# Optimization experiments

Measured on AMD Instinct MI355X. Metric: run time of the kernel, lower is better.

Reference implementation:

```python
import jax, jax.numpy as jnp
import numpy as np

L = 6                      # lmax = mmax (single resolution)
C = 128                    # sphere_channels
H = 256                    # hidden_channels
EC = 128                   # edge_channels
NG = 512                   # gaussian distance basis size
NC = (L + 1) ** 2          # 49 spherical coefficients
GP = 2 * (L + 1) ** 2      # 98 grid points
N_ATOMS = 800
N_EDGES = 8000
MAX_ELEM = 90
CUTOFF = 8.0
M_SIZES = [L - m + 1 for m in range(L + 1)]
MAXIN = L * C              # widest per-m SO2 input (m=1)


def _perm_np():
    # l-primary index of coefficient (l, m) is l*l + l + m
    idx = lambda l, m: l * l + l + m
    p = [idx(l, 0) for l in range(L + 1)]
    for m in range(1, L + 1):
        p += [idx(l, -m) for l in range(m, L + 1)]
        p += [idx(l, m) for l in range(m, L + 1)]
    return np.array(p)

_P = _perm_np()
PERM = jnp.array(_P)          # l-primary -> m-primary (x._m_primary)
INV_PERM = jnp.array(np.argsort(_P))  # m-primary -> l-primary (x._l_primary)


def silu(x):
    return x * jax.nn.sigmoid(x)


def setup_inputs() -> dict:
    key = jax.random.key(0)
    ks = iter(jax.random.split(key, 64))
    def nrm(shape, scale):
        return jax.random.normal(next(ks), shape, dtype=jnp.float32) * np.float32(scale)
    def lin(out_d, in_d):
        return nrm((out_d, in_d), 1.0 / np.sqrt(in_d))
    def so2_params(prefix):
        return {
            prefix + 'w_dist0': lin(H, EC), prefix + 'b_dist0': jnp.zeros((H,), jnp.float32),
            prefix + 'w1_m0': lin(H, M_SIZES[0] * C), prefix + 'w2_m0': lin(M_SIZES[0] * C, H),
            prefix + 'wdist_m': nrm((L, 2 * H, EC), 1.0 / np.sqrt(EC)),
            prefix + 'bdist_m': jnp.zeros((L, 2 * H), jnp.float32),
            prefix + 'w1r': nrm((L, H, MAXIN), 1.0 / np.sqrt(MAXIN)),
            prefix + 'w2r': nrm((L, MAXIN, H), 1.0 / np.sqrt(H)),
            prefix + 'w1i': nrm((L, H, MAXIN), 1.0 / np.sqrt(MAXIN)),
            prefix + 'w2i': nrm((L, MAXIN, H), 1.0 / np.sqrt(H)),
        }
    inp = dict(
        x=nrm((N_ATOMS, NC, C), 1.0),
        edge_distance=jax.random.uniform(next(ks), (N_EDGES,), jnp.float32, 0.5, CUTOFF),
        wigner=nrm((N_EDGES, NC, NC), 1.0 / np.sqrt(NC)),
        wigner_inv=nrm((N_EDGES, NC, NC), 1.0 / np.sqrt(NC)),
        to_grid_mat=nrm((GP, NC), 1.0 / np.sqrt(NC)),
        from_grid_mat=nrm((NC, GP), 1.0 / np.sqrt(GP)),
        w_dist1=lin(EC, NG), b_dist1=jnp.zeros((EC,), jnp.float32),
        src_emb=jax.random.uniform(next(ks), (MAX_ELEM, EC), jnp.float32, -0.001, 0.001),
        tgt_emb=jax.random.uniform(next(ks), (MAX_ELEM, EC), jnp.float32, -0.001, 0.001),
        w_edge1=lin(EC, EC), b_edge1=jnp.zeros((EC,), jnp.float32),
        ws1=lin(C, 2 * C), bs1=jnp.zeros((C,), jnp.float32),
        ws2=lin(C, C), bs2=jnp.zeros((C,), jnp.float32),
        ws3=lin(C, C), bs3=jnp.zeros((C,), jnp.float32),
        atomic_numbers=jax.random.randint(next(ks), (N_ATOMS,), 0, MAX_ELEM),
        edge_index=jax.random.randint(next(ks), (2, N_EDGES), 0, N_ATOMS),
    )
    inp.update(so2_params('s_'))
    inp.update(so2_params('t_'))
    return inp


def _so2_block(xr, x_edge, p):
    # SO2Block: m-primary reorder, m=0 gated MLP, per-m complex gated GEMMs, back to l-primary
    (w_dist0, b_dist0, w1_m0, w2_m0, wdist_m, bdist_m, w1r, w2r, w1i, w2i) = p
    E = xr.shape[0]
    xm = xr[:, PERM]                                   # [E, NC, C] m-primary
    n0 = M_SIZES[0]
    g0 = silu(x_edge @ w_dist0.T + b_dist0)            # [E, H]
    x0 = xm[:, :n0].reshape(E, n0 * C)
    x0 = ((x0 @ w1_m0.T) * g0) @ w2_m0.T
    outs = [x0.reshape(E, n0, C)]
    off = n0
    for m in range(1, L + 1):
        n = M_SIZES[m]; k = n * C
        blk = xm[:, off:off + 2 * n].reshape(E, 2, k)  # [E, 2(real/imag), n*C]
        ge = silu(x_edge @ wdist_m[m - 1].T + bdist_m[m - 1]).reshape(E, 2, H)
        xr_ = jnp.einsum('eik,hk->eih', blk, w1r[m - 1, :, :k]) * ge[:, 0:1]
        xr_ = jnp.einsum('eih,kh->eik', xr_, w2r[m - 1, :k])
        xi_ = jnp.einsum('eik,hk->eih', blk, w1i[m - 1, :, :k]) * ge[:, 1:2]
        xi_ = jnp.einsum('eih,kh->eik', xi_, w2i[m - 1, :k])
        out = jnp.stack([xr_[:, 0] - xi_[:, 1], xr_[:, 1] + xi_[:, 0]], axis=1)
        outs.append(out.reshape(E, 2 * n, C))
        off += 2 * n
    return jnp.concatenate(outs, axis=1)[:, INV_PERM]


def reference(x, edge_distance, wigner, wigner_inv, to_grid_mat, from_grid_mat,
              w_dist1, b_dist1, src_emb, tgt_emb, w_edge1, b_edge1,
              s_w_dist0, s_b_dist0, s_w1_m0, s_w2_m0, s_wdist_m, s_bdist_m,
              s_w1r, s_w2r, s_w1i, s_w2i,
              t_w_dist0, t_b_dist0, t_w1_m0, t_w2_m0, t_wdist_m, t_bdist_m,
              t_w1r, t_w2r, t_w1i, t_w2i,
              ws1, bs1, ws2, bs2, ws3, bs3,
              atomic_numbers, edge_index):
    # --- EdgeBlock ---
    offsets = jnp.linspace(0.0, CUTOFF, NG)
    coeff = np.float32(-0.5 / (CUTOFF / (NG - 1)) ** 2)
    basis = jnp.exp(coeff * (edge_distance[:, None] - offsets) ** 2)   # GaussianSmearing
    x_dist = basis @ w_dist1.T + b_dist1
    x_edge = silu(src_emb[atomic_numbers[edge_index[0]]]
                  + tgt_emb[atomic_numbers[edge_index[1]]] + x_dist)
    x_edge = silu(x_edge @ w_edge1.T + b_edge1)                        # [E, EC]
    # --- gather per-edge embeddings and rotate into edge frame ---
    x_src = jnp.einsum('eij,ejc->eic', wigner, x[edge_index[0]])
    x_tgt = jnp.einsum('eij,ejc->eic', wigner, x[edge_index[1]])
    # --- SO2 blocks ---
    x_src = _so2_block(x_src, x_edge, (s_w_dist0, s_b_dist0, s_w1_m0, s_w2_m0,
                                       s_wdist_m, s_bdist_m, s_w1r, s_w2r, s_w1i, s_w2i))
    x_tgt = _so2_block(x_tgt, x_edge, (t_w_dist0, t_b_dist0, t_w1_m0, t_w2_m0,
                                       t_wdist_m, t_bdist_m, t_w1r, t_w2r, t_w1i, t_w2i))
    msg = x_src + x_tgt
    # --- grid activation (x._grid_act) ---
    g = silu(jnp.einsum('gi,eic->egc', to_grid_mat, msg))
    msg = jnp.einsum('ig,egc->eic', from_grid_mat, g)
    # --- rotate back and aggregate (x._rotate_inv, x._reduce_edge) ---
    msg = jnp.einsum('eij,ejc->eic', wigner_inv, msg)
    x_msg = jax.ops.segment_sum(msg, edge_index[1], num_segments=x.shape[0])
    # --- LayerBlock point-wise spherical nonlinearity on the grid ---
    gx = jnp.einsum('gi,nic->ngc', to_grid_mat, x)
    gm = jnp.einsum('gi,nic->ngc', to_grid_mat, x_msg)
    g = jnp.concatenate([gx, gm], axis=-1)            # [N, GP, 2C]
    g = silu(g @ ws1.T + bs1)
    g = silu(g @ ws2.T + bs2)
    g = g @ ws3.T + bs3
    return jnp.einsum('ig,ngc->nic', from_grid_mat, g)
```

## Files before the change

### kernel.cpp

```cpp
#include <hip/hip_runtime.h>
#include <string.h>

#define EN 8000
#define AN 800

typedef __attribute__((ext_vector_type(8))) short bf16x8;
typedef __attribute__((ext_vector_type(4))) float f32x4;
typedef unsigned short ushort_t;
typedef unsigned int uint32;

__constant__ int c_perm[49] = {
  0,2,6,12,20,30,42,
  1,5,11,19,29,41,
  3,7,13,21,31,43,
  4,10,18,28,40,
  8,14,22,32,44,
  9,17,27,39,
  15,23,33,45,
  16,26,38,
  24,34,46,
  25,37,
  35,47,
  36,
  48
};

__device__ __forceinline__ float siluf(float x) { return x / (1.0f + __expf(-x)); }
__device__ __forceinline__ ushort_t f2bf(float f) {
  uint32 u = __float_as_uint(f);
  u += 0x7fff + ((u >> 16) & 1);
  return (ushort_t)(u >> 16);
}
__device__ __forceinline__ float bf2f(ushort_t h) {
  return __uint_as_float(((uint32)h) << 16);
}
__device__ __forceinline__ void gld16(const void* g, void* l) {
  __builtin_amdgcn_global_load_lds(
      (const __attribute__((address_space(1))) void*)g,
      (__attribute__((address_space(3))) void*)l, 16, 0, 0);
}

__global__ __launch_bounds__(256) void k_build_b2b(
    const float* __restrict__ sw2r, const float* __restrict__ sw2i,
    const float* __restrict__ tw2r, const float* __restrict__ tw2i,
    ushort_t* __restrict__ dst)
{
  long long id = (long long)blockIdx.x * 256 + threadIdx.x;
  if (id >= 5505024LL) return;
  long long base = 0; int m = 1, k = 768;
  for (; m <= 6; ++m) {
    k = (7 - m) * 128;
    long long sz = 2LL * k * 1024;
    if (id < base + sz) break;
    base += sz;
  }
  long long rem = id - base;
  int p = (int)(rem / ((long long)k * 1024));
  int cj = (int)(rem - (long long)p * k * 1024);
  int c = cj >> 10, j = cj & 1023;
  int q = j >> 8, jj = j & 255;
  const float sgn = (q & 1) ? (p ? 1.f : -1.f) : 1.f;
  const float* src = (q < 2) ? (q == 0 ? sw2r : sw2i) : (q == 2 ? tw2r : tw2i);
  dst[id] = f2bf(sgn * src[(long long)(m - 1) * 196608 + c * 256 + jj]);
}

__global__ __launch_bounds__(256) void k_build_bgcat(
    const float* __restrict__ sw0, const float* __restrict__ tw0,
    const float* __restrict__ sw4, const float* __restrict__ tw4,
    const float* __restrict__ sb0, const float* __restrict__ tb0b,
    const float* __restrict__ sbd, const float* __restrict__ tbd,
    ushort_t* __restrict__ w, float* __restrict__ b)
{
  int id = blockIdx.x * 256 + threadIdx.x;
  if (id < 851968) {
    int r = id >> 7, c = id & 127;
    float v;
    if (r < 256) v = sw0[r * 128 + c];
    else if (r < 512) v = tw0[(r - 256) * 128 + c];
    else {
      int rr = r - 512, m = rr >> 10, q = rr & 1023;
      v = (q < 512) ? sw4[m * 65536 + q * 128 + c] : tw4[m * 65536 + (q - 512) * 128 + c];
    }
    w[id] = f2bf(v);
    return;
  }
  id -= 851968;
  if (id < 6656) {
    float v;
    if (id < 256) v = sb0[id];
    else if (id < 512) v = tb0b[id - 256];
    else {
      int rr = id - 512, m = rr >> 10, q = rr & 1023;
      v = (q < 512) ? sbd[m * 512 + q] : tbd[m * 512 + (q - 512)];
    }
    b[id] = v;
  }
}

__global__ __launch_bounds__(256) void k_build_b20b(
    const float* __restrict__ sw3, const float* __restrict__ tw3,
    ushort_t* __restrict__ b20)
{
  int id = blockIdx.x * 256 + threadIdx.x;
  if (id >= 458752) return;
  int cc = id >> 9, j = id & 511;
  b20[id] = f2bf((j < 256) ? sw3[cc * 256 + j] : tw3[cc * 256 + (j - 256)]);
}

__global__ __launch_bounds__(256) void k_build_s1m(
    const float* __restrict__ sw6, const float* __restrict__ sw8,
    const float* __restrict__ tw6, const float* __restrict__ tw8,
    ushort_t* __restrict__ dst)
{
  long long id = (long long)blockIdx.x * 256 + threadIdx.x;
  if (id >= 2752512LL) return;
  long long base = 0; int m = 1, k = 768;
  for (; m <= 6; ++m) {
    k = (7 - m) * 128;
    long long sz = 1024LL * k;
    if (id < base + sz) break;
    base += sz;
  }
  long long rem = id - base;
  int s = (int)(rem / (512LL * k));
  int rr = (int)(rem - (long long)s * 512 * k);
  int r = rr / k, c = rr - r * k;
  const float* src = (r < 256) ? (s ? tw6 : sw6) : (s ? tw8 : sw8);
  int r0 = (r < 256) ? r : r - 256;
  dst[id] = f2bf(src[(long long)(m - 1) * 196608 + r0 * 768 + c]);
}

__global__ __launch_bounds__(256) void k_cvt(
    const float* __restrict__ src, ushort_t* __restrict__ dst, int n)
{
  int id = blockIdx.x * 256 + threadIdx.x;
  if (id < n) dst[id] = f2bf(src[id]);
}

__global__ __launch_bounds__(256) void k_build_tg(
    const float* __restrict__ tg, ushort_t* __restrict__ dst)
{
  int id = blockIdx.x * 256 + threadIdx.x;
  if (id >= 98 * 49) return;
  int r = id / 49, s = id - r * 49;
  dst[id] = f2bf(tg[r * 49 + c_perm[s]]);
}

__global__ __launch_bounds__(256) void k_xT(
    const float* __restrict__ x, ushort_t* __restrict__ xbT)
{
  __shared__ __align__(16) float xs[49 * 128];
  const int a = blockIdx.x, t = threadIdx.x;
  const float4* src = (const float4*)(x + (long long)a * 6272);
  float4* d = (float4*)xs;
  for (int i = t; i < 1568; i += 256) d[i] = src[i];
  __syncthreads();
  ushort_t* o = xbT + (long long)a * 8192;
  int c = t >> 1;
  int jg = (t & 1) << 2;
  #pragma unroll
  for (int u = 0; u < 4; ++u) {
    int g = jg + u;
    bf16x8 v = (bf16x8)0;
    #pragma unroll
    for (int j = 0; j < 8; ++j) {
      int jj = (g << 3) + j;
      if (jj < 49) v[j] = (short)f2bf(xs[jj * 128 + c]);
    }
    *(bf16x8*)&o[(c << 6) + (g << 3)] = v;
  }
}

__global__ __launch_bounds__(256) void k_basis(
    const float* __restrict__ dist, ushort_t* __restrict__ basis)
{
  int id = blockIdx.x * 256 + threadIdx.x;
  if (id >= EN * 512) return;
  int e = id >> 9, g = id & 511;
  const float step = 8.0f / 511.0f;
  const float coeff = -2040.0078125f;
  float df = dist[e] - (float)g * step;
  basis[id] = f2bf(expf(coeff * df * df));
}

__global__ __launch_bounds__(256) void k_emb(
    const float* __restrict__ src_emb, const float* __restrict__ tgt_emb,
    const int* __restrict__ anum, const int* __restrict__ eidx,
    const float* __restrict__ xd, ushort_t* __restrict__ out)
{
  int id = blockIdx.x * 256 + threadIdx.x;
  if (id >= EN * 128) return;
  int e = id >> 7, c = id & 127;
  int a0 = anum[eidx[e]], a1 = anum[eidx[EN + e]];
  out[id] = f2bf(siluf(src_emb[a0 * 128 + c] + tgt_emb[a1 * 128 + c] + xd[id]));
}

__global__ __launch_bounds__(256) void k_rot2(
    const float* __restrict__ wig, const ushort_t* __restrict__ xbT,
    const int* __restrict__ srcl, const int* __restrict__ tgtl,
    ushort_t* __restrict__ osrc, ushort_t* __restrict__ otgt)
{
  __shared__ short Ws[4096];
  __shared__ short Xs[8192];
  __shared__ short Xt[8192];
  const int e = blockIdx.x, tid = threadIdx.x;
  const int lane = tid & 63, wave = tid >> 6;
  const float* wge = wig + (long long)e * 2401;
  #pragma unroll
  for (int t = 0; t < 2; ++t) {
    int ci = (t << 8) + tid;
    int row = ci >> 3, g = ci & 7;
    bf16x8 v = (bf16x8)0;
    if (row < 49) {
      const float* wr = wge + c_perm[row] * 49;
      #pragma unroll
      for (int j = 0; j < 8; ++j) {
        int col = (g << 3) + j;
        if (col < 49) v[j] = (short)f2bf(wr[col]);
      }
    }
    *(bf16x8*)&Ws[(row << 6) + ((g ^ (row & 7)) << 3)] = v;
  }
  const int as = srcl[e], at = tgtl[e];
  const ushort_t* xsg = xbT + (long long)as * 8192;
  const ushort_t* xtg = xbT + (long long)at * 8192;
  #pragma unroll
  for (int t = 0; t < 4; ++t) {
    int ci = (t << 8) + tid;
    int row = ci >> 3, g = ci & 7;
    int ofs = (row << 6) + ((g ^ (row & 7)) << 3);
    *(bf16x8*)&Xs[ofs] = *(const bf16x8*)&xsg[ci << 3];
    *(bf16x8*)&Xt[ofs] = *(const bf16x8*)&xtg[ci << 3];
  }
  __syncthreads();
  const short* Xb = (wave >> 1) ? Xt : Xs;
  const int ch = (wave & 1) << 6;
  const int fr = lane & 15, g = lane >> 4;
  f32x4 acc[4][4];
  #pragma unroll
  for (int i = 0; i < 4; ++i)
    #pragma unroll
    for (int j = 0; j < 4; ++j) acc[i][j] = (f32x4){0.f, 0.f, 0.f, 0.f};
  #pragma unroll
  for (int ks = 0; ks < 2; ++ks) {
    bf16x8 af[4], bfv[4];
    int lc = (ks << 2) + g;
    #pragma unroll
    for (int i = 0; i < 4; ++i) {
      int ra = (i << 4) + fr;
      af[i] = *(const bf16x8*)&Ws[(ra << 6) + ((lc ^ (ra & 7)) << 3)];
      int rb = ch + (i << 4) + fr;
      bfv[i] = *(const bf16x8*)&Xb[(rb << 6) + ((lc ^ (rb & 7)) << 3)];
    }
    #pragma unroll
    for (int i = 0; i < 4; ++i)
      #pragma unroll
      for (int j = 0; j < 4; ++j)
        acc[i][j] = __builtin_amdgcn_mfma_f32_16x16x32_bf16(af[i], bfv[j], acc[i][j], 0, 0, 0);
  }
  const int crl = (lane >> 4) << 2, ccl = lane & 15;
  __syncthreads();
  short* Ob = (wave >> 1) ? Xt : Xs;
  #pragma unroll
  for (int i = 0; i < 4; ++i)
    #pragma unroll
    for (int r = 0; r < 4; ++r) {
      int q = (i << 4) + crl + r;
      if (q < 49) {
        #pragma unroll
        for (int j = 0; j < 4; ++j) {
          int col = ch + (j << 4) + ccl;
          Ob[(q << 7) + (((col >> 3) ^ (q & 15)) << 3) + (col & 7)] =
              (short)f2bf(acc[i][j][r]);
        }
      }
    }
  __syncthreads();
  for (int gid = tid; gid < 1568; gid += 256) {
    int half = gid >= 784;
    int c784 = half ? gid - 784 : gid;
    int row = c784 >> 4, cc = c784 & 15;
    const short* Sb = half ? Xt : Xs;
    bf16x8 v = *(const bf16x8*)&Sb[(row << 7) + ((cc ^ (row & 15)) << 3)];
    ushort_t* dst = (half ? otgt : osrc) + (long long)e * 6272 + (row << 7) + (cc << 3);
    *(bf16x8*)dst = v;
  }
}

struct GemmP {
  const ushort_t* A; const ushort_t* A2; const ushort_t* B;
  const float* bias; const ushort_t* gate; void* C;
  int a_se, a_si, pair, asplit;
  int ldb;
  int gate_ofs;
  int c_se, c_si, c_ofs;
  int ihalf, act, c_bf16;
  int M, N, K;
  int ngx, wg_base;
};
struct Grouped { GemmP d[14]; int nd; int nwg; };

__global__ __launch_bounds__(256) void gemm_g(Grouped G) {
  __shared__ short SH[16384];
  short* As = SH;
  short* Bs = SH + 8192;
  int bid;
  {
    int n = G.nwg, orig = blockIdx.x;
    int q = n >> 3, r = n & 7;
    int xcd = orig & 7, pos = orig >> 3;
    bid = (xcd < r ? xcd * (q + 1) : r * (q + 1) + (xcd - r) * q) + pos;
  }
  int di = G.nd - 1;
  for (int i = 1; i < G.nd; ++i) if (bid < G.d[i].wg_base) { di = i - 1; break; }
  const GemmP p = G.d[di];
  const int local = bid - p.wg_base;
  const int bx = local % p.ngx, by = local / p.ngx;
  const int m0 = bx << 7, n0 = by << 7;

  const int tid = threadIdx.x;
  const int lane = tid & 63, wave = tid >> 6;
  const int gl = ((lane & 3) ^ ((lane >> 3) & 3)) << 3;
  const int grow = (wave << 4) + (lane >> 2);
  const int fr = lane & 15, fkg = lane >> 4;
  const int sxor = (fr >> 1) & 3;
  const int wm = (wave >> 1) << 6, wn = (wave & 1) << 6;

  f32x4 acc[4][4];
  #pragma unroll
  for (int i = 0; i < 4; ++i)
    #pragma unroll
    for (int j = 0; j < 4; ++j) acc[i][j] = (f32x4){0.f, 0.f, 0.f, 0.f};

  long long abase;
  {
    int r0 = m0 + grow;
    abase = p.pair
        ? (long long)(r0 >> 1) * p.a_se + (long long)(r0 & 1) * p.a_si
        : (long long)r0 * p.a_se;
  }
  long long abase2;
  {
    int r1 = m0 + 64 + grow;
    abase2 = p.pair
        ? (long long)(r1 >> 1) * p.a_se + (long long)(r1 & 1) * p.a_si
        : (long long)r1 * p.a_se;
  }
  const long long bbase  = (long long)(n0 + grow) * p.ldb;
  const long long bbase2 = (long long)(n0 + 64 + grow) * p.ldb;

  const int nt = p.K >> 5;

  auto STAGE = [&](int buf, int k0) {
    const ushort_t* Ap = p.A;
    int kk = k0;
    if (p.A2 && k0 >= p.asplit) { Ap = p.A2; kk = k0 - p.asplit; }
    const int lofs = (buf << 12) + (wave << 9);
    gld16(Ap + abase + kk + gl,   &As[lofs]);
    gld16(p.B + bbase + k0 + gl,  &Bs[lofs]);
    gld16(Ap + abase2 + kk + gl,  &As[lofs + 2048]);
    gld16(p.B + bbase2 + k0 + gl, &Bs[lofs + 2048]);
  };

  STAGE(0, 0);
  int cur = 0;
  for (int t = 0; t < nt; ++t) {
    if (t + 1 < nt) {
      STAGE(cur ^ 1, (t + 1) << 5);
      asm volatile("s_waitcnt vmcnt(4)" ::: "memory");
    } else {
      asm volatile("s_waitcnt vmcnt(0)" ::: "memory");
    }
    __builtin_amdgcn_sched_barrier(0);
    __builtin_amdgcn_s_barrier();
    {
      const int bofs = cur << 12;
      bf16x8 af[4], bfv[4];
      #pragma unroll
      for (int i = 0; i < 4; ++i) {
        int ra = wm + (i << 4) + fr;
        int rb = wn + (i << 4) + fr;
        af[i]  = *(const bf16x8*)&As[bofs + (ra << 5) + ((fkg ^ sxor) << 3)];
        bfv[i] = *(const bf16x8*)&Bs[bofs + (rb << 5) + ((fkg ^ sxor) << 3)];
      }
      #pragma unroll
      for (int i = 0; i < 4; ++i)
        #pragma unroll
        for (int j = 0; j < 4; ++j)
          acc[i][j] = __builtin_amdgcn_mfma_f32_16x16x32_bf16(af[i], bfv[j], acc[i][j], 0, 0, 0);
    }
    __builtin_amdgcn_s_barrier();
    cur ^= 1;
  }

  const int crl = (lane >> 4) << 2, ccl = lane & 15;
  if (p.c_bf16) {
    #pragma unroll
    for (int mi = 0; mi < 4; ++mi)
      #pragma unroll
      for (int r = 0; r < 4; ++r) {
        int lrow = wm + mi * 16 + crl + r;
        #pragma unroll
        for (int ni = 0; ni < 4; ++ni) {
          int lcol = wn + ni * 16 + ccl;
          float v = acc[mi][ni][r];
          int gc = n0 + lcol;
          if (p.bias) v += p.bias[gc];
          if (p.act)  v = siluf(v);
          SH[(lrow << 7) + (((lcol >> 3) ^ (lrow & 15)) << 3) + (lcol & 7)] =
              (short)f2bf(v);
        }
      }
    __syncthreads();
    const int lr = tid >> 1, chalf = (tid & 1) << 6;
    int gr = m0 + lr;
    if (gr < p.M) {
      long long e; int ii;
      if (p.pair) { e = gr >> 1; ii = gr & 1; } else { e = gr; ii = 0; }
      const ushort_t* grw = p.gate ? p.gate + e * 6656 + p.gate_ofs : nullptr;
      #pragma unroll
      for (int j = 0; j < 8; ++j) {
        int lcol = chalf + (j << 3);
        bf16x8 v = *(const bf16x8*)&SH[(lr << 7) + (((lcol >> 3) ^ (lr & 15)) << 3)];
        int gc = n0 + lcol;
        if (grw) {
          bf16x8 g8 = *(const bf16x8*)&grw[gc];
          #pragma unroll
          for (int q2 = 0; q2 < 8; ++q2)
            v[q2] = (short)f2bf(bf2f((ushort_t)v[q2]) * bf2f((ushort_t)g8[q2]));
        }
        int par = (p.ihalf && gc >= 256) ? (1 - ii) : ii;
        long long co = e * (long long)p.c_se + (long long)par * p.c_si + p.c_ofs + gc;
        *(bf16x8*)&((ushort_t*)p.C)[co] = v;
      }
    }
  } else {
    #pragma unroll
    for (int mi = 0; mi < 4; ++mi) {
      #pragma unroll
      for (int r = 0; r < 4; ++r) {
        int gr = m0 + wm + mi * 16 + crl + r;
        if (gr >= p.M) continue;
        long long e = gr;
        float* crow = (float*)p.C + e * (long long)p.c_se + p.c_ofs;
        #pragma unroll
        for (int ni = 0; ni < 4; ++ni) {
          int gc = n0 + wn + ni * 16 + ccl;
          if (gc >= p.N) continue;
          float v = acc[mi][ni][r];
          if (p.bias) v += p.bias[gc];
          if (p.act)  v = siluf(v);
          crow[gc] = v;
        }
      }
    }
  }
}

struct GridP {
  const float* A; const ushort_t* B; void* C; const float* bias;
  int b_ib, c_ib;
  int M, K, permA, act, c_bf16;
};

#define LDW 40

__global__ __launch_bounds__(256) void gridmm(GridP p) {
  __shared__ short As[128 * LDW];
  __shared__ short Bs[128 * LDW];
  const int e = blockIdx.x;
  const int tid = threadIdx.x;
  const int srow = tid >> 1, sk = (tid & 1) << 4;
  const int lane = tid & 63, wave = tid >> 6;
  const int wm = (wave >> 1) << 6, wn = (wave & 1) << 6;
  const int fr = lane & 15, fk = (lane >> 4) << 3;

  f32x4 acc[4][4];
  #pragma unroll
  for (int i = 0; i < 4; ++i)
    #pragma unroll
    for (int j = 0; j < 4; ++j) acc[i][j] = (f32x4){0.f, 0.f, 0.f, 0.f};

  const ushort_t* bp0 = p.B + (long long)e * p.b_ib;

  for (int k0 = 0; k0 < p.K; k0 += 32) {
    {
      bf16x8 lo = (bf16x8)0, hi = (bf16x8)0;
      if (srow < p.M) {
        const float* ar = p.A + srow * p.K;
        #pragma unroll
        for (int j = 0; j < 8; ++j) {
          int col = k0 + sk + j;
          float v = 0.f;
          if (col < p.K) v = ar[p.permA ? c_perm[col] : col];
          lo[j] = (short)f2bf(v);
        }
        #pragma unroll
        for (int j = 0; j < 8; ++j) {
          int col = k0 + sk + 8 + j;
          float v = 0.f;
          if (col < p.K) v = ar[p.permA ? c_perm[col] : col];
          hi[j] = (short)f2bf(v);
        }
      }
      *(bf16x8*)&As[srow * LDW + sk] = lo;
      *(bf16x8*)&As[srow * LDW + sk + 8] = hi;
    }
    {
      const int c = tid & 127, kq = tid >> 7;
      #pragma unroll
      for (int i = 0; i < 8; ++i) {
        int kk = kq * 16 + i * 2;
        int k1 = k0 + kk, k2 = k1 + 1;
        uint32 v0 = (k1 < p.K) ? (uint32)bp0[(long long)k1 * 128 + c] : 0u;
        uint32 v1 = (k2 < p.K) ? (uint32)bp0[(long long)k2 * 128 + c] : 0u;
        *(uint32*)&Bs[c * LDW + kk] = v0 | (v1 << 16);
      }
    }
    __syncthreads();
    bf16x8 af[4], bfv[4];
    #pragma unroll
    for (int i = 0; i < 4; ++i) {
      af[i]  = *(const bf16x8*)(&As[(wm + i * 16 + fr) * LDW + fk]);
      bfv[i] = *(const bf16x8*)(&Bs[(wn + i * 16 + fr) * LDW + fk]);
    }
    #pragma unroll
    for (int i = 0; i < 4; ++i)
      #pragma unroll
      for (int j = 0; j < 4; ++j)
        acc[i][j] = __builtin_amdgcn_mfma_f32_16x16x32_bf16(af[i], bfv[j], acc[i][j], 0, 0, 0);
    __syncthreads();
  }

  const int crl = (lane >> 4) << 2, ccl = lane & 15;
  #pragma unroll
  for (int mi = 0; mi < 4; ++mi) {
    #pragma unroll
    for (int r = 0; r < 4; ++r) {
      int gr = wm + mi * 16 + crl + r;
      if (gr >= p.M) continue;
      #pragma unroll
      for (int ni = 0; ni < 4; ++ni) {
        int c = wn + ni * 16 + ccl;
        float v = acc[mi][ni][r];
        if (p.bias) v += p.bias[c];
        if (p.act)  v = siluf(v);
        long long co = (long long)e * p.c_ib + gr * 128 + c;
        if (p.c_bf16) ((ushort_t*)p.C)[co] = f2bf(v);
        else          ((float*)p.C)[co] = v;
      }
    }
  }
}

#define SWZ8(cg, r) (((cg) ^ ((r) & 7)) & 7)
#define SWZ16(cg, r) (((cg) & 8) | (((cg) ^ (r)) & 7))

__global__ __launch_bounds__(256, 2) void k_grid(
    const ushort_t* __restrict__ tgb, const ushort_t* __restrict__ fgb,
    const float* __restrict__ wigv, const ushort_t* __restrict__ msgp,
    ushort_t* __restrict__ msg3)
{
  __shared__ short Abuf[8192];
  __shared__ short Bsh[8192];
  __shared__ short Ps[16384];
  const int e = blockIdx.x, tid = threadIdx.x;
  const int lane = tid & 63, wv = tid >> 6;
  const int fr = lane & 15, fk = (lane >> 4) << 3;
  const int crl = (lane >> 4) << 2, ccl = lane & 15;
  const ushort_t* me = msgp + (long long)e * 6272;

  for (int gid = tid; gid < 896; gid += 256) {
    int r = gid >> 3, cg = gid & 7;
    bf16x8 v = (bf16x8)0;
    if (r < 98) {
      #pragma unroll
      for (int j = 0; j < 8; ++j) {
        int col = (cg << 3) + j;
        if (col < 49) v[j] = (short)tgb[r * 49 + col];
      }
    }
    *(bf16x8*)&Abuf[(r << 6) + (SWZ8(cg, r) << 3)] = v;
  }
  for (int gid = tid; gid < 1024; gid += 256) {
    int kg = gid >> 7, c = gid & 127;
    bf16x8 v = (bf16x8)0;
    #pragma unroll
    for (int j = 0; j < 8; ++j) {
      int k = (kg << 3) + j;
      if (k < 49) v[j] = (short)me[k * 128 + c];
    }
    *(bf16x8*)&Bsh[(c << 6) + (SWZ8(kg, c) << 3)] = v;
  }
  {
    int c = tid >> 1, gg = 14 + (tid & 1);
    *(bf16x8*)&Ps[(c << 7) + (SWZ16(gg, c) << 3)] = (bf16x8)0;
  }
  __syncthreads();

  {
    f32x4 acc[7][2];
    #pragma unroll
    for (int i = 0; i < 7; ++i) { acc[i][0] = (f32x4){0,0,0,0}; acc[i][1] = (f32x4){0,0,0,0}; }
    #pragma unroll
    for (int k0 = 0; k0 < 64; k0 += 32) {
      int cg = (k0 + fk) >> 3;
      int br0 = ((2 * wv) << 4) + fr, br1 = ((2 * wv + 1) << 4) + fr;
      bf16x8 bf0 = *(const bf16x8*)&Bsh[(br0 << 6) + (SWZ8(cg, br0) << 3)];
      bf16x8 bf1 = *(const bf16x8*)&Bsh[(br1 << 6) + (SWZ8(cg, br1) << 3)];
      #pragma unroll
      for (int rt = 0; rt < 7; ++rt) {
        int ar = (rt << 4) + fr;
        bf16x8 af = *(const bf16x8*)&Abuf[(ar << 6) + (SWZ8(cg, ar) << 3)];
        acc[rt][0] = __builtin_amdgcn_mfma_f32_16x16x32_bf16(af, bf0, acc[rt][0], 0, 0, 0);
        acc[rt][1] = __builtin_amdgcn_mfma_f32_16x16x32_bf16(af, bf1, acc[rt][1], 0, 0, 0);
      }
    }
    #pragma unroll
    for (int rt = 0; rt < 7; ++rt)
      #pragma unroll
      for (int cj = 0; cj < 2; ++cj) {
        int c = ((2 * wv + cj) << 4) + ccl;
        #pragma unroll
        for (int r = 0; r < 4; ++r) {
          int g = (rt << 4) + crl + r;
          Ps[(c << 7) + (SWZ16(g >> 3, c) << 3) + (g & 7)] =
              (short)f2bf(siluf(acc[rt][cj][r]));
        }
      }
  }
  __syncthreads();
  for (int gid = tid; gid < 1024; gid += 256) {
    int r = gid >> 4, cg = gid & 15;
    bf16x8 v = (bf16x8)0;
    if (r < 49) {
      #pragma unroll
      for (int j = 0; j < 8; ++j) {
        int col = (cg << 3) + j;
        if (col < 98) v[j] = (short)fgb[r * 98 + col];
      }
    }
    *(bf16x8*)&Abuf[(r << 7) + (SWZ16(cg, r) << 3)] = v;
  }
  __syncthreads();

  {
    f32x4 acc[4][2];
    #pragma unroll
    for (int i = 0; i < 4; ++i) { acc[i][0] = (f32x4){0,0,0,0}; acc[i][1] = (f32x4){0,0,0,0}; }
    #pragma unroll
    for (int k0 = 0; k0 < 128; k0 += 32) {
      int cg = (k0 + fk) >> 3;
      int br0 = ((2 * wv) << 4) + fr, br1 = ((2 * wv + 1) << 4) + fr;
      bf16x8 bf0 = *(const bf16x8*)&Ps[(br0 << 7) + (SWZ16(cg, br0) << 3)];
      bf16x8 bf1 = *(const bf16x8*)&Ps[(br1 << 7) + (SWZ16(cg, br1) << 3)];
      #pragma unroll
      for (int rt = 0; rt < 4; ++rt) {
        int ar = (rt << 4) + fr;
        bf16x8 af = *(const bf16x8*)&Abuf[(ar << 7) + (SWZ16(cg, ar) << 3)];
        acc[rt][0] = __builtin_amdgcn_mfma_f32_16x16x32_bf16(af, bf0, acc[rt][0], 0, 0, 0);
        acc[rt][1] = __builtin_amdgcn_mfma_f32_16x16x32_bf16(af, bf1, acc[rt][1], 0, 0, 0);
      }
    }
    #pragma unroll
    for (int rt = 0; rt < 4; ++rt)
      #pragma unroll
      for (int cj = 0; cj < 2; ++cj) {
        int c = ((2 * wv + cj) << 4) + ccl;
        #pragma unroll
        for (int r = 0; r < 4; ++r) {
          int q = (rt << 4) + crl + r;
          Bsh[(c << 6) + (SWZ8(q >> 3, c) << 3) + (q & 7)] = (short)f2bf(acc[rt][cj][r]);
        }
      }
  }
  __syncthreads();
  {
    const float* we = wigv + (long long)e * 2401;
    for (int gid = tid; gid < 512; gid += 256) {
      int r = gid >> 3, cg = gid & 7;
      bf16x8 v = (bf16x8)0;
      if (r < 49) {
        #pragma unroll
        for (int j = 0; j < 8; ++j) {
          int col = (cg << 3) + j;
          if (col < 49) v[j] = (short)f2bf(we[r * 49 + col]);
        }
      }
      *(bf16x8*)&Abuf[(r << 6) + (SWZ8(cg, r) << 3)] = v;
    }
  }
  __syncthreads();

  {
    f32x4 acc[4][2];
    #pragma unroll
    for (int i = 0; i < 4; ++i) { acc[i][0] = (f32x4){0,0,0,0}; acc[i][1] = (f32x4){0,0,0,0}; }
    #pragma unroll
    for (int k0 = 0; k0 < 64; k0 += 32) {
      int cg = (k0 + fk) >> 3;
      int br0 = ((2 * wv) << 4) + fr, br1 = ((2 * wv + 1) << 4) + fr;
      bf16x8 bf0 = *(const bf16x8*)&Bsh[(br0 << 6) + (SWZ8(cg, br0) << 3)];
      bf16x8 bf1 = *(const bf16x8*)&Bsh[(br1 << 6) + (SWZ8(cg, br1) << 3)];
      #pragma unroll
      for (int rt = 0; rt < 4; ++rt) {
        int ar = (rt << 4) + fr;
        bf16x8 af = *(const bf16x8*)&Abuf[(ar << 6) + (SWZ8(cg, ar) << 3)];
        acc[rt][0] = __builtin_amdgcn_mfma_f32_16x16x32_bf16(af, bf0, acc[rt][0], 0, 0, 0);
        acc[rt][1] = __builtin_amdgcn_mfma_f32_16x16x32_bf16(af, bf1, acc[rt][1], 0, 0, 0);
      }
    }
    #pragma unroll
    for (int rt = 0; rt < 4; ++rt)
      #pragma unroll
      for (int r = 0; r < 4; ++r) {
        int gi = (rt << 4) + crl + r;
        if (gi < 49) {
          #pragma unroll
          for (int cj = 0; cj < 2; ++cj) {
            int c = ((2 * wv + cj) << 4) + ccl;
            Ps[(gi << 7) + (((c >> 3) ^ (gi & 15)) << 3) + (c & 7)] =
                (short)f2bf(acc[rt][cj][r]);
          }
        }
      }
    __syncthreads();
    ushort_t* oe = msg3 + (long long)e * 6272;
    for (int gid = tid; gid < 784; gid += 256) {
      int row = gid >> 4, cc = gid & 15;
      bf16x8 v = *(const bf16x8*)&Ps[(row << 7) + ((cc ^ (row & 15)) << 3)];
      *(bf16x8*)&oe[(row << 7) + (cc << 3)] = v;
    }
  }
}

__global__ __launch_bounds__(256) void k_zeroi(int* __restrict__ p, int n) {
  int id = blockIdx.x * 256 + threadIdx.x;
  if (id < n) p[id] = 0;
}

__global__ __launch_bounds__(256) void k_deg(
    const int* __restrict__ tgt, int* __restrict__ deg) {
  int e = blockIdx.x * 256 + threadIdx.x;
  if (e < EN) atomicAdd(&deg[tgt[e]], 1);
}

__global__ __launch_bounds__(1024) void k_prefix(
    const int* __restrict__ deg, int* __restrict__ base) {
  __shared__ int s[1024];
  int t = threadIdx.x;
  s[t] = (t < AN) ? deg[t] : 0;
  __syncthreads();
  for (int ofs = 1; ofs < 1024; ofs <<= 1) {
    int u = (t >= ofs) ? s[t - ofs] : 0;
    __syncthreads();
    s[t] += u;
    __syncthreads();
  }
  if (t < AN) base[t + 1] = s[t];
  if (t == 0) base[0] = 0;
}

__global__ __launch_bounds__(256) void k_fill(
    const int* __restrict__ tgt, const int* __restrict__ base,
    int* __restrict__ list) {
  const int a = blockIdx.x, t = threadIdx.x;
  const int lane = t & 63, w = t >> 6;
  __shared__ int wtot[4];
  __shared__ int runbase;
  if (t == 0) runbase = base[a];
  __syncthreads();
  for (int i0 = 0; i0 < EN; i0 += 256) {
    int e = i0 + t;
    bool m = (e < EN) && (tgt[e] == a);
    unsigned long long bal = __ballot(m);
    if (lane == 0) wtot[w] = __popcll(bal);
    __syncthreads();
    int wbase = 0;
    for (int j = 0; j < w; ++j) wbase += wtot[j];
    int tot = wtot[0] + wtot[1] + wtot[2] + wtot[3];
    if (m) {
      int off = __popcll(bal & ((1ull << lane) - 1ull));
      list[runbase + wbase + off] = e;
    }
    __syncthreads();
    if (t == 0) runbase += tot;
    __syncthreads();
  }
}

__global__ __launch_bounds__(256) void k_gather4(
    const ushort_t* __restrict__ msg3, const int* __restrict__ base,
    const int* __restrict__ list, float* __restrict__ xmsg,
    int e0, int ce, int accum)
{
  const int a = blockIdx.x, part = blockIdx.y, t = threadIdx.x;
  if (t >= 196) return;
  const int b0 = base[a], b1 = base[a + 1];
  const int co = part * 1568 + t * 8;
  float a8[8];
  #pragma unroll
  for (int u = 0; u < 8; ++u) a8[u] = 0.f;
  for (int i = b0; i < b1; ++i) {
    int e = list[i];
    if (e < e0 || e >= e0 + ce) continue;
    bf16x8 v = *(const bf16x8*)&msg3[(long long)(e - e0) * 6272 + co];
    #pragma unroll
    for (int u = 0; u < 8; ++u) a8[u] += bf2f((ushort_t)v[u]);
  }
  float* o = xmsg + (long long)a * 6272 + co;
  if (accum) {
    #pragma unroll
    for (int u = 0; u < 8; ++u) o[u] += a8[u];
  } else {
    float4 lo = make_float4(a8[0], a8[1], a8[2], a8[3]);
    float4 hi = make_float4(a8[4], a8[5], a8[6], a8[7]);
    *(float4*)o = lo;
    *(float4*)(o + 4) = hi;
  }
}

extern "C" void kernel_launch(void* const* d_in, const int* in_sizes, int n_in,
                              void* d_out, int out_size, void* d_ws, size_t ws_size,
                              hipStream_t stream) {
  const float* x         = (const float*)d_in[0];
  const float* edist     = (const float*)d_in[1];
  const float* wigner    = (const float*)d_in[2];
  const float* wiginv    = (const float*)d_in[3];
  const float* to_grid   = (const float*)d_in[4];
  const float* from_grid = (const float*)d_in[5];
  const float* w_dist1   = (const float*)d_in[6];
  const float* b_dist1   = (const float*)d_in[7];
  const float* src_emb   = (const float*)d_in[8];
  const float* tgt_emb   = (const float*)d_in[9];
  const float* w_edge1   = (const float*)d_in[10];
  const float* b_edge1   = (const float*)d_in[11];
  const float* ws1       = (const float*)d_in[12];
  const float* bs1       = (const float*)d_in[13];
  const float* ws2       = (const float*)d_in[14];
  const float* bs2       = (const float*)d_in[15];
  const float* ws3       = (const float*)d_in[16];
  const float* bs3       = (const float*)d_in[17];
  const int*   anum      = (const int*)d_in[18];
  const int*   eidx      = (const int*)d_in[19];
  const float* sw[10]; const float* tw[10];
  for (int i = 0; i < 10; ++i) {
    sw[i] = (const float*)d_in[20 + i];
    tw[i] = (const float*)d_in[30 + i];
  }
  float* outp = (float*)d_out;

  char* wsb = (char*)d_ws;
  size_t off = 0;
  auto alloc = [&](long long nbytes) {
    char* p = wsb + off; off += (size_t)((nbytes + 63) & ~63LL); return p;
  };
  ushort_t* x_edge  = (ushort_t*)alloc((8000LL + 128) * 128 * 2);
  ushort_t* b2ab    = (ushort_t*)alloc(5505024LL * 2);
  ushort_t* bgcw    = (ushort_t*)alloc(851968LL * 2);
  float*    bgcb    = (float*)alloc(6656 * 4);
  ushort_t* b20b    = (ushort_t*)alloc(458752LL * 2);
  ushort_t* s1m0b   = (ushort_t*)alloc(458752LL * 2);
  ushort_t* s1mb    = (ushort_t*)alloc(2752512LL * 2);
  ushort_t* wd1b    = (ushort_t*)alloc(65536 * 2);
  ushort_t* we1b    = (ushort_t*)alloc(16384 * 2);
  ushort_t* ws1b    = (ushort_t*)alloc(32768 * 2);
  ushort_t* ws2b    = (ushort_t*)alloc(16384 * 2);
  ushort_t* ws3b    = (ushort_t*)alloc(16384 * 2);
  ushort_t* tgb     = (ushort_t*)alloc(4802 * 2);
  ushort_t* fgb     = (ushort_t*)alloc(4802 * 2);
  float*    xmsg    = (float*)alloc(5017600LL * 4);
  ushort_t* xmsgb   = (ushort_t*)alloc((5017600LL + 16384) * 2);
  ushort_t* xb      = (ushort_t*)alloc((5017600LL + 16384) * 2);
  ushort_t* xbT     = (ushort_t*)alloc(6553600LL * 2);
  ushort_t* basis   = (ushort_t*)alloc((8000LL + 128) * 512 * 2);
  float*    x_dist  = (float*)alloc(1024000LL * 4);
  ushort_t* x_distb = (ushort_t*)alloc((8000LL + 128) * 128 * 2);
  int*      deg     = (int*)alloc(800 * 4);
  int*      sbase   = (int*)alloc(801 * 4);
  int*      elist   = (int*)alloc(8000 * 4);
  const size_t fixedB = off;
  char* arena = wsb + off;

  static const int ces[6] = {8000, 4000, 2000, 1000, 500, 250};
  static const int cas[6] = {800, 800, 800, 400, 200, 100};
  int ce = 250, ca = 100;
  for (int i = 0; i < 6; ++i) {
    long long ne = (long long)ces[i] * 76544 + 64LL * 50688;
    long long na = (long long)cas[i] * 87808 + 64LL * 512;
    long long need = (long long)fixedB + (ne > na ? ne : na);
    if (need <= (long long)ws_size) { ce = ces[i]; ca = cas[i]; break; }
  }

  char* ap = arena;
  ushort_t* xrot_s = (ushort_t*)ap;  ap += (long long)(ce + 64) * 12544;
  ushort_t* xrot_t = (ushort_t*)ap;  ap += (long long)(ce + 64) * 12544;
  ushort_t* tb0    = (ushort_t*)ap;  ap += (long long)(ce + 64) * 1024;
  ushort_t* tbm    = (ushort_t*)ap;  ap += (long long)(ce + 64) * 24576;
  ushort_t* msgp   = (ushort_t*)ap;  ap += (long long)ce * 12544;
  ushort_t* gate   = (ushort_t*)ap;
  ushort_t* msg3   = (ushort_t*)arena;
  char* bp = arena;
  ushort_t* hb = (ushort_t*)bp;  bp += (long long)ca * 49 * 256;
  ushort_t* g1 = (ushort_t*)bp;  bp += ((long long)ca * 98 + 64) * 256;
  ushort_t* g2 = (ushort_t*)bp;  bp += ((long long)ca * 98 + 64) * 256;
  ushort_t* g3 = (ushort_t*)bp;

  long long ofs2[7][2], s1ofs[7][2];
  { long long cur = 0, cur1 = 0;
    for (int m = 1; m <= 6; ++m) {
      int k = (7 - m) * 128;
      ofs2[m][0] = cur; cur += (long long)k * 1024;
      ofs2[m][1] = cur; cur += (long long)k * 1024;
      s1ofs[m][0] = cur1; cur1 += 512LL * k;
      s1ofs[m][1] = cur1; cur1 += 512LL * k;
    } }

  auto D0 = []() { GemmP p; memset(&p, 0, sizeof(p)); p.asplit = 1 << 30; return p; };
  auto finalize = [&](Grouped& G) {
    int base = 0;
    for (int i = 0; i < G.nd; ++i) {
      GemmP& p = G.d[i];
      p.ngx = (p.M + 127) >> 7;
      int ngy = (p.N + 127) >> 7;
      p.wg_base = base;
      base += p.ngx * ngy;
    }
    G.nwg = base;
    gemm_g<<<base, 256, 0, stream>>>(G);
  };
  auto run1 = [&](GemmP p) { Grouped G; G.d[0] = p; G.nd = 1; finalize(G); };
  auto rungrid = [&](const float* A, int M, int K, int permA,
                     const ushort_t* B, int b_ib, void* C, int c_ib,
                     const float* bias, int act, int c_bf16, int nb) {
    GridP p;
    p.A = A; p.B = B; p.C = C; p.bias = bias;
    p.b_ib = b_ib; p.c_ib = c_ib;
    p.M = M; p.K = K; p.permA = permA; p.act = act; p.c_bf16 = c_bf16;
    gridmm<<<nb, 256, 0, stream>>>(p);
  };
  auto cvt = [&](const float* s, ushort_t* d, int n) {
    k_cvt<<<(n + 255) / 256, 256, 0, stream>>>(s, d, n);
  };

  k_build_b2b<<<(5505024 + 255) / 256, 256, 0, stream>>>(sw[7], sw[9], tw[7], tw[9], b2ab);
  k_build_bgcat<<<(858624 + 255) / 256, 256, 0, stream>>>(
      sw[0], tw[0], sw[4], tw[4], sw[1], tw[1], sw[5], tw[5], bgcw, bgcb);
  k_build_b20b<<<(458752 + 255) / 256, 256, 0, stream>>>(sw[3], tw[3], b20b);
  k_build_s1m<<<(2752512 + 255) / 256, 256, 0, stream>>>(sw[6], sw[8], tw[6], tw[8], s1mb);
  cvt(sw[2], s1m0b, 229376);
  cvt(tw[2], s1m0b + 229376, 229376);
  cvt(w_dist1, wd1b, 65536);
  cvt(w_edge1, we1b, 16384);
  cvt(ws1, ws1b, 32768);
  cvt(ws2, ws2b, 16384);
  cvt(ws3, ws3b, 16384);
  cvt(from_grid, fgb, 4802);
  k_build_tg<<<(4802 + 255) / 256, 256, 0, stream>>>(to_grid, tgb);
  cvt(x, xb, 5017600);
  k_xT<<<AN, 256, 0, stream>>>(x, xbT);

  k_zeroi<<<4, 256, 0, stream>>>(deg, 800);
  k_deg<<<(EN + 255) / 256, 256, 0, stream>>>(eidx + EN, deg);
  k_prefix<<<1, 1024, 0, stream>>>(deg, sbase);
  k_fill<<<AN, 256, 0, stream>>>(eidx + EN, sbase, elist);

  k_basis<<<(EN * 512 + 255) / 256, 256, 0, stream>>>(edist, basis);
  { GemmP p = D0();
    p.A = basis; p.a_se = 512; p.B = wd1b; p.ldb = 512; p.bias = b_dist1;
    p.C = x_dist; p.c_se = 128; p.M = EN; p.N = 128; p.K = 512;
    run1(p); }
  k_emb<<<(EN * 128 + 255) / 256, 256, 0, stream>>>(src_emb, tgt_emb, anum, eidx,
                                                    x_dist, x_distb);
  { GemmP p = D0();
    p.A = x_distb; p.a_se = 128; p.B = we1b; p.ldb = 128; p.bias = b_edge1;
    p.act = 1; p.C = x_edge; p.c_se = 128; p.c_bf16 = 1;
    p.M = EN; p.N = 128; p.K = 128;
    run1(p); }

  static const int offq[7] = {0, 7, 19, 29, 37, 43, 47};

  for (int e0 = 0; e0 < EN; e0 += ce) {
    const int c = ce;
    k_rot2<<<c, 256, 0, stream>>>(wigner + (long long)e0 * 2401, xbT,
                                  eidx + e0, eidx + EN + e0, xrot_s, xrot_t);
    { GemmP p = D0();
      p.A = x_edge + (long long)e0 * 128; p.a_se = 128;
      p.B = bgcw; p.ldb = 128; p.bias = bgcb; p.act = 1;
      p.C = gate; p.c_se = 6656; p.c_bf16 = 1;
      p.M = c; p.N = 6656; p.K = 128;
      run1(p); }
    { Grouped G; G.nd = 14;
      for (int s = 0; s < 2; ++s) {
        GemmP p = D0();
        p.A = s ? xrot_t : xrot_s; p.a_se = 6272;
        p.B = s1m0b + (long long)s * 229376; p.ldb = 896;
        p.gate = gate; p.gate_ofs = s * 256;
        p.C = tb0; p.c_se = 512; p.c_ofs = s * 256; p.c_bf16 = 1;
        p.M = c; p.N = 256; p.K = 896;
        G.d[s] = p;
      }
      int di = 2;
      for (int m = 1; m <= 6; ++m) {
        const int k = (7 - m) * 128, off2 = offq[m];
        for (int s = 0; s < 2; ++s) {
          GemmP p = D0();
          p.A = (s ? xrot_t : xrot_s) + off2 * 128;
          p.a_se = 6272; p.a_si = k; p.pair = 1;
          p.B = s1mb + s1ofs[m][s]; p.ldb = k;
          p.gate = gate; p.gate_ofs = 512 + (m - 1) * 1024 + s * 512;
          p.C = tbm; p.c_se = 12288; p.c_si = 1024;
          p.c_ofs = (m - 1) * 2048 + s * 512;
          p.ihalf = 1; p.c_bf16 = 1;
          p.M = 2 * c; p.N = 512; p.K = k;
          G.d[di++] = p;
        }
      }
      finalize(G); }
    { Grouped G; G.nd = 13;
      { GemmP p = D0();
        p.A = tb0; p.a_se = 512;
        p.B = b20b; p.ldb = 512;
        p.C = msgp; p.c_se = 6272; p.c_bf16 = 1;
        p.M = c; p.N = 896; p.K = 512;
        G.d[0] = p; }
      int di = 1;
      for (int m = 1; m <= 6; ++m) {
        const int n = 7 - m, k = n * 128, off2 = offq[m];
        for (int pp = 0; pp < 2; ++pp) {
          GemmP p = D0();
          p.A = tbm + (m - 1) * 2048 + pp * 1024; p.a_se = 12288;
          p.B = b2ab + ofs2[m][pp]; p.ldb = 1024;
          p.C = msgp; p.c_se = 6272; p.c_ofs = (off2 + (pp ? n : 0)) * 128; p.c_bf16 = 1;
          p.M = c; p.N = k; p.K = 1024;
          G.d[di++] = p;
        }
      }
      finalize(G); }
    k_grid<<<c, 256, 0, stream>>>(tgb, fgb, wiginv + (long long)e0 * 2401, msgp, msg3);
    k_gather4<<<dim3(AN, 4), 256, 0, stream>>>(msg3, sbase, elist, xmsg, e0, c, e0 > 0);
  }

  cvt(xmsg, xmsgb, 5017600);

  for (int a0 = 0; a0 < AN; a0 += ca) {
    { GemmP p = D0();
      p.A = xb + (long long)a0 * 6272; p.A2 = xmsgb + (long long)a0 * 6272;
      p.a_se = 128; p.asplit = 128;
      p.B = ws1b; p.ldb = 256;
      p.C = hb; p.c_se = 128; p.c_bf16 = 1;
      p.M = ca * 49; p.N = 128; p.K = 256;
      run1(p); }
    rungrid(to_grid, 98, 49, 0, hb, 6272, g1, 12544, bs1, 1, 1, ca);
    { GemmP p = D0();
      p.A = g1; p.a_se = 128;
      p.B = ws2b; p.ldb = 128; p.bias = bs2; p.act = 1;
      p.C = g2; p.c_se = 128; p.c_bf16 = 1;
      p.M = ca * 98; p.N = 128; p.K = 128;
      run1(p); }
    { GemmP p = D0();
      p.A = g2; p.a_se = 128;
      p.B = ws3b; p.ldb = 128; p.bias = bs3;
      p.C = g3; p.c_se = 128; p.c_bf16 = 1;
      p.M = ca * 98; p.N = 128; p.K = 128;
      run1(p); }
    rungrid(from_grid, 49, 98, 0, g3, 12544, outp + (long long)a0 * 6272, 6272,
            nullptr, 0, 0, ca);
  }
}
```

Before: 1.636 ms.

## Fuse per-m gate projection into SO2 GEMM epilogue and batch weight conversions

The m>0 gate values were produced by a separate GEMM over the full 6656-wide gate matrix and stored to a global buffer. They are now computed inside the grouped SO2 GEMM epilogue with a small extra MFMA over x_edge and the gate weights held in a new shared-memory tile. The standalone gate GEMM shrinks to the 512 m=0 columns, which removes a large intermediate write and read and lowers the per-chunk workspace so larger chunks fit. Several fp32-to-bf16 conversion launches are merged into one multi-segment kernel. The cost is extra LDS use per block (possibly lower occupancy) and recomputing the gate once per paired row tile.

```diff
diff --git a/kernel.cpp b/kernel.cpp
--- a/kernel.cpp
+++ b/kernel.cpp
@@ -128,6 +128,21 @@
   const float* src = (r < 256) ? (s ? tw6 : sw6) : (s ? tw8 : sw8);
   int r0 = (r < 256) ? r : r - 256;
   dst[id] = f2bf(src[(long long)(m - 1) * 196608 + r0 * 768 + c]);
+}
+
+struct CvtM {
+  const float* s[9];
+  ushort_t* d[9];
+  long long start[10];
+};
+__global__ __launch_bounds__(256) void k_cvt_multi(CvtM P) {
+  long long id = (long long)blockIdx.x * 256 + threadIdx.x;
+  if (id >= P.start[9]) return;
+  int seg = 0;
+  #pragma unroll
+  for (int i = 1; i < 9; ++i) if (id >= P.start[i]) seg = i;
+  long long o = id - P.start[seg];
+  P.d[seg][o] = f2bf(P.s[seg][o]);
 }
 
 __global__ __launch_bounds__(256) void k_cvt(
@@ -290,9 +305,12 @@
 struct GemmP {
   const ushort_t* A; const ushort_t* A2; const ushort_t* B;
   const float* bias; const ushort_t* gate; void* C;
+  const ushort_t* gxe;
+  const ushort_t* gw;
+  const float* gb;
   int a_se, a_si, pair, asplit;
   int ldb;
-  int gate_ofs;
+  int gate_ofs, gse;
   int c_se, c_si, c_ofs;
   int ihalf, act, c_bf16;
   int M, N, K;
@@ -302,6 +320,7 @@
 
 __global__ __launch_bounds__(256) void gemm_g(Grouped G) {
   __shared__ short SH[16384];
+  __shared__ short GH[8192];
   short* As = SH;
   short* Bs = SH + 8192;
   int bid;
@@ -412,18 +431,76 @@
         }
       }
     __syncthreads();
+
+    if (p.gxe) {
+      f32x4 gacc[4][4];
+      #pragma unroll
+      for (int i = 0; i < 4; ++i)
+        #pragma unroll
+        for (int j = 0; j < 4; ++j) gacc[i][j] = (f32x4){0.f, 0.f, 0.f, 0.f};
+      #pragma unroll
+      for (int ks = 0; ks < 4; ++ks) {
+        #pragma unroll
+        for (int t = 0; t < 2; ++t) {
+          int row = (t << 6) + grow;
+          int ar = m0 + row;
+          int eidx = p.pair ? (ar >> 1) : ar;
+          bf16x8 av = *(const bf16x8*)&p.gxe[(long long)eidx * 128 + (ks << 5) + gl];
+          *(bf16x8*)&GH[(row << 5) + ((lane & 3) << 3)] = av;
+          bf16x8 bv = *(const bf16x8*)&p.gw[
+              (long long)(p.gate_ofs + n0 + row) * 128 + (ks << 5) + gl];
+          *(bf16x8*)&GH[4096 + (row << 5) + ((lane & 3) << 3)] = bv;
+        }
+        __syncthreads();
+        bf16x8 af[4], bfv[4];
+        #pragma unroll
+        for (int i = 0; i < 4; ++i) {
+          int ra = wm + (i << 4) + fr;
+          int rb = wn + (i << 4) + fr;
+          af[i]  = *(const bf16x8*)&GH[(ra << 5) + ((fkg ^ sxor) << 3)];
+          bfv[i] = *(const bf16x8*)&GH[4096 + (rb << 5) + ((fkg ^ sxor) << 3)];
+        }
+        #pragma unroll
+        for (int i = 0; i < 4; ++i)
+          #pragma unroll
+          for (int j = 0; j < 4; ++j)
+            gacc[i][j] = __builtin_amdgcn_mfma_f32_16x16x32_bf16(af[i], bfv[j], gacc[i][j], 0, 0, 0);
+        __syncthreads();
+      }
+      #pragma unroll
+      for (int mi = 0; mi < 4; ++mi)
+        #pragma unroll
+        for (int r = 0; r < 4; ++r) {
+          int lrow = wm + mi * 16 + crl + r;
+          int gr = p.pair ? (lrow >> 1) : (lrow & 63);
+          #pragma unroll
+          for (int ni = 0; ni < 4; ++ni) {
+            int lcol = wn + ni * 16 + ccl;
+            float gv = siluf(gacc[mi][ni][r] + p.gb[p.gate_ofs + n0 + lcol]);
+            GH[(gr << 7) + lcol] = (short)f2bf(gv);
+          }
+        }
+      __syncthreads();
+    }
+
     const int lr = tid >> 1, chalf = (tid & 1) << 6;
     int gr = m0 + lr;
     if (gr < p.M) {
       long long e; int ii;
       if (p.pair) { e = gr >> 1; ii = gr & 1; } else { e = gr; ii = 0; }
-      const ushort_t* grw = p.gate ? p.gate + e * 6656 + p.gate_ofs : nullptr;
+      const ushort_t* grw = p.gate ? p.gate + e * p.gse + p.gate_ofs : nullptr;
       #pragma unroll
       for (int j = 0; j < 8; ++j) {
         int lcol = chalf + (j << 3);
         bf16x8 v = *(const bf16x8*)&SH[(lr << 7) + (((lcol >> 3) ^ (lr & 15)) << 3)];
         int gc = n0 + lcol;
-        if (grw) {
+        if (p.gxe) {
+          int gr2 = p.pair ? (lr >> 1) : lr;
+          bf16x8 g8 = *(const bf16x8*)&GH[(gr2 << 7) + lcol];
+          #pragma unroll
+          for (int q2 = 0; q2 < 8; ++q2)
+            v[q2] = (short)f2bf(bf2f((ushort_t)v[q2]) * bf2f((ushort_t)g8[q2]));
+        } else if (grw) {
           bf16x8 g8 = *(const bf16x8*)&grw[gc];
           #pragma unroll
           for (int q2 = 0; q2 < 8; ++q2)
@@ -886,7 +963,7 @@
   static const int cas[6] = {800, 800, 800, 400, 200, 100};
   int ce = 250, ca = 100;
   for (int i = 0; i < 6; ++i) {
-    long long ne = (long long)ces[i] * 76544 + 64LL * 50688;
+    long long ne = (long long)ces[i] * 66048 + 64LL * 50688;
     long long na = (long long)cas[i] * 87808 + 64LL * 512;
     long long need = (long long)fixedB + (ne > na ? ne : na);
     if (need <= (long long)ws_size) { ce = ces[i]; ca = cas[i]; break; }
@@ -939,25 +1016,23 @@
     p.M = M; p.K = K; p.permA = permA; p.act = act; p.c_bf16 = c_bf16;
     gridmm<<<nb, 256, 0, stream>>>(p);
   };
-  auto cvt = [&](const float* s, ushort_t* d, int n) {
-    k_cvt<<<(n + 255) / 256, 256, 0, stream>>>(s, d, n);
-  };
 
   k_build_b2b<<<(5505024 + 255) / 256, 256, 0, stream>>>(sw[7], sw[9], tw[7], tw[9], b2ab);
   k_build_bgcat<<<(858624 + 255) / 256, 256, 0, stream>>>(
       sw[0], tw[0], sw[4], tw[4], sw[1], tw[1], sw[5], tw[5], bgcw, bgcb);
   k_build_b20b<<<(458752 + 255) / 256, 256, 0, stream>>>(sw[3], tw[3], b20b);
   k_build_s1m<<<(2752512 + 255) / 256, 256, 0, stream>>>(sw[6], sw[8], tw[6], tw[8], s1mb);
-  cvt(sw[2], s1m0b, 229376);
-  cvt(tw[2], s1m0b + 229376, 229376);
-  cvt(w_dist1, wd1b, 65536);
-  cvt(w_edge1, we1b, 16384);
-  cvt(ws1, ws1b, 32768);
-  cvt(ws2, ws2b, 16384);
-  cvt(ws3, ws3b, 16384);
-  cvt(from_grid, fgb, 4802);
+  {
+    CvtM P;
+    const float* ss[9] = { sw[2], tw[2], w_dist1, w_edge1, ws1, ws2, ws3, from_grid, x };
+    ushort_t* dd[9] = { s1m0b, s1m0b + 229376, wd1b, we1b, ws1b, ws2b, ws3b, fgb, xb };
+    long long nn[9] = { 229376, 229376, 65536, 16384, 32768, 16384, 16384, 4802, 5017600 };
+    long long cur = 0;
+    for (int i = 0; i < 9; ++i) { P.s[i] = ss[i]; P.d[i] = dd[i]; P.start[i] = cur; cur += nn[i]; }
+    P.start[9] = cur;
+    k_cvt_multi<<<(int)((cur + 255) / 256), 256, 0, stream>>>(P);
+  }
   k_build_tg<<<(4802 + 255) / 256, 256, 0, stream>>>(to_grid, tgb);
-  cvt(x, xb, 5017600);
   k_xT<<<AN, 256, 0, stream>>>(x, xbT);
 
   k_zeroi<<<4, 256, 0, stream>>>(deg, 800);
@@ -987,15 +1062,15 @@
     { GemmP p = D0();
       p.A = x_edge + (long long)e0 * 128; p.a_se = 128;
       p.B = bgcw; p.ldb = 128; p.bias = bgcb; p.act = 1;
-      p.C = gate; p.c_se = 6656; p.c_bf16 = 1;
-      p.M = c; p.N = 6656; p.K = 128;
+      p.C = gate; p.c_se = 512; p.c_bf16 = 1;
+      p.M = c; p.N = 512; p.K = 128;
       run1(p); }
     { Grouped G; G.nd = 14;
       for (int s = 0; s < 2; ++s) {
         GemmP p = D0();
         p.A = s ? xrot_t : xrot_s; p.a_se = 6272;
         p.B = s1m0b + (long long)s * 229376; p.ldb = 896;
-        p.gate = gate; p.gate_ofs = s * 256;
+        p.gate = gate; p.gate_ofs = s * 256; p.gse = 512;
         p.C = tb0; p.c_se = 512; p.c_ofs = s * 256; p.c_bf16 = 1;
         p.M = c; p.N = 256; p.K = 896;
         G.d[s] = p;
@@ -1008,7 +1083,9 @@
           p.A = (s ? xrot_t : xrot_s) + off2 * 128;
           p.a_se = 6272; p.a_si = k; p.pair = 1;
           p.B = s1mb + s1ofs[m][s]; p.ldb = k;
-          p.gate = gate; p.gate_ofs = 512 + (m - 1) * 1024 + s * 512;
+          p.gxe = x_edge + (long long)e0 * 128;
+          p.gw = bgcw; p.gb = bgcb;
+          p.gate_ofs = 512 + (m - 1) * 1024 + s * 512;
           p.C = tbm; p.c_se = 12288; p.c_si = 1024;
           p.c_ofs = (m - 1) * 2048 + s * 512;
           p.ihalf = 1; p.c_bf16 = 1;
@@ -1041,7 +1118,7 @@
     k_gather4<<<dim3(AN, 4), 256, 0, stream>>>(msg3, sbase, elist, xmsg, e0, c, e0 > 0);
   }
 
-  cvt(xmsg, xmsgb, 5017600);
+  k_cvt<<<(5017600 + 255) / 256, 256, 0, stream>>>(xmsg, xmsgb, 5017600);
 
   for (int a0 = 0; a0 < AN; a0 += ca) {
     { GemmP p = D0();
```

Measured after the change: 2.339 ms. 1.43x slower.
